# Kernel tuning notes

Measured on AMD Instinct MI355X. Metric: run time of the kernel, lower is better.

The kernel has to match this reference:

```python
import jax, jax.numpy as jnp
import numpy as np

N_NODES = 100000
K = 10
ALPHA = 0.1


def _gcn_norm(ei, n):
    # add self loops (PyG APPNP default: add_self_loops=True, gcn_norm)
    loops = jnp.arange(n, dtype=ei.dtype)
    src = jnp.concatenate([ei[0], loops])
    dst = jnp.concatenate([ei[1], loops])
    ones = jnp.ones(src.shape[0], dtype=jnp.float32)
    deg = jax.ops.segment_sum(ones, dst, num_segments=n)
    dinv = jnp.where(deg > 0, jax.lax.rsqrt(deg), 0.0)
    norm = dinv[src] * dinv[dst]  # [E+N]
    return src, dst, norm


def reference(x, ei, W1, b1, W2, b2):
    n = x.shape[0]
    # MLP encoder (dropout is identity in eval mode)
    h = jax.nn.relu(x @ W1 + b1)
    h = h @ W2 + b2  # [N, out_c]
    src, dst, norm = _gcn_norm(ei, n)
    h0 = h
    for _ in range(K):
        msg = norm[:, None] * h[src]                      # gather [E+N, out_c]
        agg = jax.ops.segment_sum(msg, dst, num_segments=n)  # scatter-add
        h = (1.0 - ALPHA) * agg + ALPHA * h0
    return h


def setup_inputs() -> dict:
    key = jax.random.key(0)
    k1, k2, k3, k4 = jax.random.split(key, 4)
    in_c, hidden, out_c = 512, 256, 64
    E = 3200000
    x = jax.random.normal(k1, (N_NODES, in_c), dtype=jnp.float32)
    ei = jax.random.randint(k2, (2, E), 0, N_NODES, dtype=jnp.int64)
    s1 = 1.0 / np.sqrt(in_c)
    s2 = 1.0 / np.sqrt(hidden)
    W1 = jax.random.uniform(k3, (in_c, hidden), jnp.float32, -s1, s1)
    b1 = jnp.zeros((hidden,), jnp.float32)
    W2 = jax.random.uniform(k4, (hidden, out_c), jnp.float32, -s2, s2)
    b2 = jnp.zeros((out_c,), jnp.float32)
    return {"x": x, "ei": ei, "W1": W1, "b1": b1, "W2": W2, "b2": b2}
```

## Files before the change

### kernel.cpp

```cpp
#include <hip/hip_runtime.h>


typedef unsigned short u16;
typedef unsigned int   u32;
typedef __bf16    bfx8  __attribute__((ext_vector_type(8)));
typedef _Float16  h16x8 __attribute__((ext_vector_type(8)));
typedef float     f32x4 __attribute__((ext_vector_type(4)));

#define CAP 4096
#define EPB 16384
#define NBMAX 1792

__device__ __forceinline__ u16 f2bf(float f) {
    u32 u = __float_as_uint(f);
    u += 0x7fffu + ((u >> 16) & 1u);
    return (u16)(u >> 16);
}


__global__ __launch_bounds__(256) void binscat_kernel(
        const int* __restrict__ src, const int* __restrict__ dst,
        int* __restrict__ gcur, u32* __restrict__ binned, int E, int NB) {
    __shared__ int cnt[NBMAX];
    int tid = threadIdx.x;
#pragma unroll
    for (int j = 0; j < NBMAX / 256; ++j) cnt[tid + j * 256] = 0;
    __syncthreads();
    int e0 = blockIdx.x * EPB;
    for (int r = 0; r < EPB / 256; ++r) {
        int i = e0 + r * 256 + tid;
        if (i < E) atomicAdd(&cnt[dst[i] >> 6], 1);
    }
    __syncthreads();
    for (int j = 0; j < NBMAX / 256; ++j) {
        int b = tid + j * 256;
        if (b < NB) {
            int c = cnt[b];
            cnt[b] = (c > 0) ? atomicAdd(&gcur[b], c) : 0;
        }
    }
    __syncthreads();
    for (int r = 0; r < EPB / 256; ++r) {
        int i = e0 + r * 256 + tid;
        if (i < E) {
            int d = dst[i];
            int s = src[i];
            int bb = d >> 6;
            int p = atomicAdd(&cnt[bb], 1);
            if (p < CAP) binned[(size_t)bb * CAP + p] = ((u32)(d & 63) << 17) | (u32)s;
        }
    }
}


__global__ __launch_bounds__(256) void bucket_scan_kernel(
        const int* __restrict__ gcur, int* __restrict__ bbase,
        int* __restrict__ rp, int N, int NB) {
    __shared__ int tsum[256];
    int tid = threadIdx.x;
    int loc[7];
    int run = 0;
#pragma unroll
    for (int j = 0; j < 7; ++j) {
        int b = tid * 7 + j;
        int v = 0;
        if (b < NB) { v = gcur[b]; if (v > CAP) v = CAP; }
        loc[j] = run;
        run += v;
    }
    tsum[tid] = run;
    __syncthreads();
    for (int off = 1; off < 256; off <<= 1) {
        int t = (tid >= off) ? tsum[tid - off] : 0;
        __syncthreads();
        tsum[tid] += t;
        __syncthreads();
    }
    int texcl = tsum[tid] - run;
#pragma unroll
    for (int j = 0; j < 7; ++j) {
        int b = tid * 7 + j;
        if (b < NB) bbase[b] = texcl + loc[j];
    }
    if (tid == 255) rp[N] = tsum[255];
}


__global__ __launch_bounds__(256) void buildcsr_kernel(
        const u32* __restrict__ binned, const int* __restrict__ gcur,
        const int* __restrict__ bbase, int* __restrict__ rp,
        float* __restrict__ dinv, int* __restrict__ csr, int N) {
    __shared__ u32 eb[CAP];
    __shared__ int lcsr[CAP];
    __shared__ int ncnt[64];
    __shared__ int lcur[64];
    int b = blockIdx.x;
    int tid = threadIdx.x;
    int cnt = gcur[b]; if (cnt > CAP) cnt = CAP;
    int base = bbase[b];
    if (tid < 64) ncnt[tid] = 0;
    __syncthreads();
    for (int idx = tid; idx < cnt; idx += 256) {
        u32 v = binned[(size_t)b * CAP + idx];
        eb[idx] = v;
        atomicAdd(&ncnt[v >> 17], 1);
    }
    __syncthreads();
    if (tid < 64) {
        int c = ncnt[tid];
        int s = c;
#pragma unroll
        for (int off = 1; off < 64; off <<= 1) {
            int t = __shfl_up(s, off);
            if (tid >= off) s += t;
        }
        int excl = s - c;
        lcur[tid] = excl;
        int node = b * 64 + tid;
        if (node < N) {
            rp[node] = base + excl;
            dinv[node] = rsqrtf(1.0f + (float)c);
        }
    }
    __syncthreads();
    for (int idx = tid; idx < cnt; idx += 256) {
        u32 v = eb[idx];
        int p = atomicAdd(&lcur[v >> 17], 1);
        lcsr[p] = (int)(v & 0x1FFFFu);
    }
    __syncthreads();
    for (int idx = tid; idx < cnt; idx += 256)
        csr[base + idx] = lcsr[idx];
}


__global__ void prepw1_kernel(const float* __restrict__ W1, u16* __restrict__ W1t) {
    int id = blockIdx.x * 256 + threadIdx.x;
    int k = id >> 8, n = id & 255;
    W1t[n * 512 + k] = f2bf(W1[id]);
}

__global__ void prepw2_kernel(const float* __restrict__ W2, u16* __restrict__ W2t) {
    int id = blockIdx.x * 256 + threadIdx.x;
    int k = id >> 6, n = id & 63;
    W2t[n * 256 + k] = f2bf(W2[id]);
}


__global__ __launch_bounds__(256) void mlp_kernel(
        const float* __restrict__ x, const u16* __restrict__ W1t,
        const float* __restrict__ b1, const u16* __restrict__ W2t,
        const float* __restrict__ b2, const float* __restrict__ dinv,
        float* __restrict__ h0, _Float16* __restrict__ hA, int N) {
    __shared__ char lds[65536];
    u16* xs  = (u16*)lds;
    u16* w1s = (u16*)(lds + 5120);
    u16* h1s = (u16*)lds;
    u16* w2s = (u16*)(lds + 32768);

    const int tid  = threadIdx.x;
    const int wave = tid >> 6;
    const int lane = tid & 63;
    const int lq   = lane >> 4;
    const int lr   = lane & 15;
    const int blockRow = blockIdx.x * 64;

    f32x4 acc[4][4];
#pragma unroll
    for (int a = 0; a < 4; ++a)
#pragma unroll
        for (int b = 0; b < 4; ++b) acc[a][b] = (f32x4){0.f, 0.f, 0.f, 0.f};

    for (int kk = 0; kk < 512; kk += 32) {
        __syncthreads();
        {
            int r = tid >> 2, c = (tid & 3) << 3;
            int gr = blockRow + r;
            float v[8];
            if (gr < N) {
                const float* p = x + (size_t)gr * 512 + kk + c;
                float4 u0 = *(const float4*)p;
                float4 u1 = *(const float4*)(p + 4);
                v[0]=u0.x; v[1]=u0.y; v[2]=u0.z; v[3]=u0.w;
                v[4]=u1.x; v[5]=u1.y; v[6]=u1.z; v[7]=u1.w;
            } else {
#pragma unroll
                for (int j = 0; j < 8; ++j) v[j] = 0.f;
            }
            u32 pk[4];
#pragma unroll
            for (int j = 0; j < 4; ++j)
                pk[j] = (u32)f2bf(v[2*j]) | ((u32)f2bf(v[2*j+1]) << 16);
            uint4 st = make_uint4(pk[0], pk[1], pk[2], pk[3]);
            *(uint4*)&xs[r * 40 + c] = st;
        }
        {
            const uint4* p = (const uint4*)(W1t + (size_t)tid * 512 + kk);
            uint4* q = (uint4*)&w1s[tid * 40];
            q[0] = p[0]; q[1] = p[1]; q[2] = p[2]; q[3] = p[3];
        }
        __syncthreads();
        bfx8 fa[4], fb[4];
#pragma unroll
        for (int mt = 0; mt < 4; ++mt)
            fa[mt] = *(bfx8*)&xs[(mt * 16 + lr) * 40 + lq * 8];
#pragma unroll
        for (int nt = 0; nt < 4; ++nt)
            fb[nt] = *(bfx8*)&w1s[(wave * 64 + nt * 16 + lr) * 40 + lq * 8];
#pragma unroll
        for (int mt = 0; mt < 4; ++mt)
#pragma unroll
            for (int nt = 0; nt < 4; ++nt)
                acc[mt][nt] = __builtin_amdgcn_mfma_f32_16x16x32_bf16(
                    fa[mt], fb[nt], acc[mt][nt], 0, 0, 0);
    }
    __syncthreads();

#pragma unroll
    for (int nt = 0; nt < 4; ++nt) {
        int col = wave * 64 + nt * 16 + lr;
        float bb = b1[col];
#pragma unroll
        for (int mt = 0; mt < 4; ++mt)
#pragma unroll
            for (int r = 0; r < 4; ++r) {
                int row = mt * 16 + lq * 4 + r;
                float v = acc[mt][nt][r] + bb;
                v = v > 0.f ? v : 0.f;
                h1s[row * 256 + col] = f2bf(v);
            }
    }
    {
        int nn = tid >> 2, seg = (tid & 3) * 64;
        const uint4* p = (const uint4*)(W2t + nn * 256 + seg);
        uint4* q = (uint4*)&w2s[nn * 256 + seg];
#pragma unroll
        for (int j = 0; j < 8; ++j) q[j] = p[j];
    }
    __syncthreads();

    f32x4 acc2[4];
#pragma unroll
    for (int a = 0; a < 4; ++a) acc2[a] = (f32x4){0.f, 0.f, 0.f, 0.f};
    for (int kk = 0; kk < 256; kk += 32) {
        bfx8 a = *(bfx8*)&h1s[(wave * 16 + lr) * 256 + kk + lq * 8];
#pragma unroll
        for (int nt = 0; nt < 4; ++nt) {
            bfx8 b = *(bfx8*)&w2s[(nt * 16 + lr) * 256 + kk + lq * 8];
            acc2[nt] = __builtin_amdgcn_mfma_f32_16x16x32_bf16(a, b, acc2[nt], 0, 0, 0);
        }
    }
#pragma unroll
    for (int nt = 0; nt < 4; ++nt) {
        int col = nt * 16 + lr;
        float bb = b2[col];
#pragma unroll
        for (int r = 0; r < 4; ++r) {
            int row = wave * 16 + lq * 4 + r;
            int gr = blockRow + row;
            if (gr < N) {
                float v = acc2[nt][r] + bb;
                size_t idx = (size_t)gr * 64 + col;
                h0[idx] = v;
                hA[idx] = (_Float16)(v * dinv[gr]);
            }
        }
    }
}


template <typename OUTT>
__global__ __launch_bounds__(256) void prop_kernel(
        const _Float16* __restrict__ hs, const float* __restrict__ h0,
        const float* __restrict__ dinv, const int* __restrict__ rp,
        const int* __restrict__ csr, OUTT* __restrict__ hout, int N) {
    int t = blockIdx.x * 256 + threadIdx.x;
    int i = t >> 3;
    int l = t & 7;
    if (i >= N) return;
    int beg = rp[i], end = rp[i + 1];
    const _Float16* hb = hs + l * 8;
    h16x8 self = *(const h16x8*)(hb + (size_t)i * 64);
    float a[8];
#pragma unroll
    for (int j = 0; j < 8; ++j) a[j] = (float)self[j];
    int e = beg;
    for (; e + 1 < end; e += 2) {
        int s0 = csr[e], s1 = csr[e + 1];
        h16x8 g0 = *(const h16x8*)(hb + (size_t)s0 * 64);
        h16x8 g1 = *(const h16x8*)(hb + (size_t)s1 * 64);
#pragma unroll
        for (int j = 0; j < 8; ++j) a[j] += (float)g0[j];
#pragma unroll
        for (int j = 0; j < 8; ++j) a[j] += (float)g1[j];
    }
    if (e < end) {
        int s0 = csr[e];
        h16x8 g0 = *(const h16x8*)(hb + (size_t)s0 * 64);
#pragma unroll
        for (int j = 0; j < 8; ++j) a[j] += (float)g0[j];
    }
    float dv = dinv[i];
    float c1 = 0.9f * dv;
    const float* h0p = h0 + (size_t)i * 64 + l * 8;
    float o[8];
#pragma unroll
    for (int j = 0; j < 8; ++j) o[j] = fmaf(c1, a[j], 0.1f * h0p[j]);
    if constexpr (sizeof(OUTT) == 2) {
        h16x8 ov;
#pragma unroll
        for (int j = 0; j < 8; ++j) ov[j] = (_Float16)(dv * o[j]);
        *(h16x8*)(hout + (size_t)i * 64 + l * 8) = ov;
    } else {
        float4* q = (float4*)(hout + (size_t)i * 64 + l * 8);
        q[0] = make_float4(o[0], o[1], o[2], o[3]);
        q[1] = make_float4(o[4], o[5], o[6], o[7]);
    }
}


extern "C" void kernel_launch(void* const* d_in, const int* in_sizes, int n_in,
                              void* d_out, int out_size, void* d_ws, size_t ws_size,
                              hipStream_t stream) {
    const float* x  = (const float*)d_in[0];
    const int*   ei = (const int*)d_in[1];
    const float* W1 = (const float*)d_in[2];
    const float* b1 = (const float*)d_in[3];
    const float* W2 = (const float*)d_in[4];
    const float* b2 = (const float*)d_in[5];
    const int N = in_sizes[0] / 512;
    const int E = in_sizes[1] / 2;
    const int NB = (N + 63) / 64;
    const int* src = ei;
    const int* dst = ei + E;

    char* w = (char*)d_ws;
    size_t off = 0;
    auto alloc = [&](size_t bytes) -> char* {
        char* p = w + off;
        off = (off + bytes + 1023) & ~(size_t)1023;
        return p;
    };
    int*      gcur  = (int*)alloc((size_t)NB * 4);
    int*      bbase = (int*)alloc((size_t)NB * 4);
    int*      rp    = (int*)alloc(((size_t)N + 1) * 4);
    float*    dinv  = (float*)alloc((size_t)N * 4);
    int*      csr   = (int*)alloc((size_t)E * 4);
    u32*      binned= (u32*)alloc((size_t)NB * CAP * 4);
    u16*      W1t   = (u16*)alloc(512 * 256 * 2);
    u16*      W2t   = (u16*)alloc(256 * 64 * 2);
    float*    h0    = (float*)alloc((size_t)N * 64 * 4);
    _Float16* hA    = (_Float16*)alloc((size_t)N * 64 * 2);
    _Float16* hB    = (_Float16*)alloc((size_t)N * 64 * 2);

    hipMemsetAsync(gcur, 0, (size_t)NB * 4, stream);
    binscat_kernel<<<(E + EPB - 1) / EPB, 256, 0, stream>>>(src, dst, gcur, binned, E, NB);
    bucket_scan_kernel<<<1, 256, 0, stream>>>(gcur, bbase, rp, N, NB);
    buildcsr_kernel<<<NB, 256, 0, stream>>>(binned, gcur, bbase, rp, dinv, csr, N);
    prepw1_kernel<<<512, 256, 0, stream>>>(W1, W1t);
    prepw2_kernel<<<64, 256, 0, stream>>>(W2, W2t);
    mlp_kernel<<<(N + 63) / 64, 256, 0, stream>>>(x, W1t, b1, W2t, b2, dinv, h0, hA, N);

    const _Float16* pin = hA;
    int grid = (N * 8 + 255) / 256;
    for (int it = 0; it < 9; ++it) {
        _Float16* pout = (it & 1) ? hA : hB;
        prop_kernel<_Float16><<<grid, 256, 0, stream>>>(pin, h0, dinv, rp, csr, pout, N);
        pin = pout;
    }
    prop_kernel<float><<<grid, 256, 0, stream>>>(pin, h0, dinv, rp, csr, (float*)d_out, N);
}
```

Measured before the change: 1.089 ms.

## Sort nodes by degree, double-buffer MLP tiles, store h0 in fp16, unroll gathers

Adds a degree histogram and counting-sort permutation so propagation threads that share a wavefront handle nodes of similar degree, which reduces divergence from uneven neighbour loops. The MLP first-layer loop is double-buffered so global loads for the next K-tile overlap the MFMA work on the current one. W2 is now read directly from global memory instead of being staged in LDS, and the h1 row stride is padded. h0 is stored in fp16, halving its traffic in every propagation pass at some cost in precision. The gather loop is unrolled by four to keep more loads in flight. The permuted node order may hurt locality of the output writes.

```diff
diff --git a/kernel.cpp b/kernel.cpp
--- a/kernel.cpp
+++ b/kernel.cpp
@@ -89,7 +89,8 @@
 __global__ __launch_bounds__(256) void buildcsr_kernel(
         const u32* __restrict__ binned, const int* __restrict__ gcur,
         const int* __restrict__ bbase, int* __restrict__ rp,
-        float* __restrict__ dinv, int* __restrict__ csr, int N) {
+        float* __restrict__ dinv, int* __restrict__ csr,
+        int* __restrict__ dhist, int N) {
     __shared__ u32 eb[CAP];
     __shared__ int lcsr[CAP];
     __shared__ int ncnt[64];
@@ -120,6 +121,8 @@
         if (node < N) {
             rp[node] = base + excl;
             dinv[node] = rsqrtf(1.0f + (float)c);
+            int dg = c > 127 ? 127 : c;
+            atomicAdd(&dhist[dg], 1);
         }
     }
     __syncthreads();
@@ -134,6 +137,44 @@
 }
 
 
+__global__ void dscan_kernel(const int* __restrict__ dhist, int* __restrict__ dcur) {
+    __shared__ int s[128];
+    int tid = threadIdx.x;
+    int v = dhist[tid];
+    s[tid] = v;
+    __syncthreads();
+    for (int off = 1; off < 128; off <<= 1) {
+        int t = (tid >= off) ? s[tid - off] : 0;
+        __syncthreads();
+        s[tid] += t;
+        __syncthreads();
+    }
+    dcur[tid] = s[tid] - v;
+}
+
+__global__ __launch_bounds__(256) void dplace_kernel(
+        const int* __restrict__ rp, int* __restrict__ dcur,
+        int* __restrict__ perm, int N) {
+    __shared__ int cnt[128];
+    __shared__ int base[128];
+    int tid = threadIdx.x;
+    if (tid < 128) cnt[tid] = 0;
+    __syncthreads();
+    int i = blockIdx.x * 256 + tid;
+    int deg = 0, lpos = 0;
+    bool valid = i < N;
+    if (valid) {
+        deg = rp[i + 1] - rp[i];
+        if (deg > 127) deg = 127;
+        lpos = atomicAdd(&cnt[deg], 1);
+    }
+    __syncthreads();
+    if (tid < 128) base[tid] = cnt[tid] ? atomicAdd(&dcur[tid], cnt[tid]) : 0;
+    __syncthreads();
+    if (valid) perm[base[deg] + lpos] = i;
+}
+
+
 __global__ void prepw1_kernel(const float* __restrict__ W1, u16* __restrict__ W1t) {
     int id = blockIdx.x * 256 + threadIdx.x;
     int k = id >> 8, n = id & 255;
@@ -151,12 +192,8 @@
         const float* __restrict__ x, const u16* __restrict__ W1t,
         const float* __restrict__ b1, const u16* __restrict__ W2t,
         const float* __restrict__ b2, const float* __restrict__ dinv,
-        float* __restrict__ h0, _Float16* __restrict__ hA, int N) {
-    __shared__ char lds[65536];
-    u16* xs  = (u16*)lds;
-    u16* w1s = (u16*)(lds + 5120);
-    u16* h1s = (u16*)lds;
-    u16* w2s = (u16*)(lds + 32768);
+        _Float16* __restrict__ h0h, _Float16* __restrict__ hA, int N) {
+    __shared__ __align__(16) char lds[51200];
 
     const int tid  = threadIdx.x;
     const int wave = tid >> 6;
@@ -165,57 +202,72 @@
     const int lr   = lane & 15;
     const int blockRow = blockIdx.x * 64;
 
+    const int sr = tid >> 2;
+    const int sc = (tid & 3) << 3;
+
+    float xv[8];
+    uint4 wv[4];
+    auto load_tile = [&](int ks) {
+        int kk = ks * 32;
+        int gr = blockRow + sr;
+        if (gr < N) {
+            const float* p = x + (size_t)gr * 512 + kk + sc;
+            float4 a0 = *(const float4*)p;
+            float4 a1 = *(const float4*)(p + 4);
+            xv[0]=a0.x; xv[1]=a0.y; xv[2]=a0.z; xv[3]=a0.w;
+            xv[4]=a1.x; xv[5]=a1.y; xv[6]=a1.z; xv[7]=a1.w;
+        } else {
+#pragma unroll
+            for (int j = 0; j < 8; ++j) xv[j] = 0.f;
+        }
+        const uint4* q = (const uint4*)(W1t + (size_t)tid * 512 + kk);
+        wv[0]=q[0]; wv[1]=q[1]; wv[2]=q[2]; wv[3]=q[3];
+    };
+    auto store_tile = [&](int buf) {
+        u16* xsb = (u16*)(lds + buf * 5120);
+        u32 pk[4];
+#pragma unroll
+        for (int j = 0; j < 4; ++j)
+            pk[j] = (u32)f2bf(xv[2*j]) | ((u32)f2bf(xv[2*j+1]) << 16);
+        *(uint4*)&xsb[sr * 40 + sc] = make_uint4(pk[0], pk[1], pk[2], pk[3]);
+        u16* w1b = (u16*)(lds + 10240 + buf * 20480);
+        uint4* qq = (uint4*)&w1b[tid * 40];
+        qq[0]=wv[0]; qq[1]=wv[1]; qq[2]=wv[2]; qq[3]=wv[3];
+    };
+
     f32x4 acc[4][4];
 #pragma unroll
     for (int a = 0; a < 4; ++a)
 #pragma unroll
         for (int b = 0; b < 4; ++b) acc[a][b] = (f32x4){0.f, 0.f, 0.f, 0.f};
 
-    for (int kk = 0; kk < 512; kk += 32) {
-        __syncthreads();
-        {
-            int r = tid >> 2, c = (tid & 3) << 3;
-            int gr = blockRow + r;
-            float v[8];
-            if (gr < N) {
-                const float* p = x + (size_t)gr * 512 + kk + c;
-                float4 u0 = *(const float4*)p;
-                float4 u1 = *(const float4*)(p + 4);
-                v[0]=u0.x; v[1]=u0.y; v[2]=u0.z; v[3]=u0.w;
-                v[4]=u1.x; v[5]=u1.y; v[6]=u1.z; v[7]=u1.w;
-            } else {
-#pragma unroll
-                for (int j = 0; j < 8; ++j) v[j] = 0.f;
-            }
-            u32 pk[4];
-#pragma unroll
-            for (int j = 0; j < 4; ++j)
-                pk[j] = (u32)f2bf(v[2*j]) | ((u32)f2bf(v[2*j+1]) << 16);
-            uint4 st = make_uint4(pk[0], pk[1], pk[2], pk[3]);
-            *(uint4*)&xs[r * 40 + c] = st;
-        }
-        {
-            const uint4* p = (const uint4*)(W1t + (size_t)tid * 512 + kk);
-            uint4* q = (uint4*)&w1s[tid * 40];
-            q[0] = p[0]; q[1] = p[1]; q[2] = p[2]; q[3] = p[3];
-        }
-        __syncthreads();
+    load_tile(0);
+    store_tile(0);
+    __syncthreads();
+    for (int ks = 0; ks < 16; ++ks) {
+        int buf = ks & 1;
+        if (ks < 15) load_tile(ks + 1);
+        const u16* xsb = (const u16*)(lds + buf * 5120);
+        const u16* w1b = (const u16*)(lds + 10240 + buf * 20480);
         bfx8 fa[4], fb[4];
 #pragma unroll
         for (int mt = 0; mt < 4; ++mt)
-            fa[mt] = *(bfx8*)&xs[(mt * 16 + lr) * 40 + lq * 8];
+            fa[mt] = *(const bfx8*)&xsb[(mt * 16 + lr) * 40 + lq * 8];
 #pragma unroll
         for (int nt = 0; nt < 4; ++nt)
-            fb[nt] = *(bfx8*)&w1s[(wave * 64 + nt * 16 + lr) * 40 + lq * 8];
+            fb[nt] = *(const bfx8*)&w1b[(wave * 64 + nt * 16 + lr) * 40 + lq * 8];
 #pragma unroll
         for (int mt = 0; mt < 4; ++mt)
 #pragma unroll
             for (int nt = 0; nt < 4; ++nt)
                 acc[mt][nt] = __builtin_amdgcn_mfma_f32_16x16x32_bf16(
                     fa[mt], fb[nt], acc[mt][nt], 0, 0, 0);
-    }
-    __syncthreads();
-
+        __syncthreads();
+        if (ks < 15) store_tile(buf ^ 1);
+        __syncthreads();
+    }
+
+    u16* h1s = (u16*)lds;
 #pragma unroll
     for (int nt = 0; nt < 4; ++nt) {
         int col = wave * 64 + nt * 16 + lr;
@@ -227,15 +279,8 @@
                 int row = mt * 16 + lq * 4 + r;
                 float v = acc[mt][nt][r] + bb;
                 v = v > 0.f ? v : 0.f;
-                h1s[row * 256 + col] = f2bf(v);
+                h1s[row * 264 + col] = f2bf(v);
             }
-    }
-    {
-        int nn = tid >> 2, seg = (tid & 3) * 64;
-        const uint4* p = (const uint4*)(W2t + nn * 256 + seg);
-        uint4* q = (uint4*)&w2s[nn * 256 + seg];
-#pragma unroll
-        for (int j = 0; j < 8; ++j) q[j] = p[j];
     }
     __syncthreads();
 
@@ -243,10 +288,10 @@
 #pragma unroll
     for (int a = 0; a < 4; ++a) acc2[a] = (f32x4){0.f, 0.f, 0.f, 0.f};
     for (int kk = 0; kk < 256; kk += 32) {
-        bfx8 a = *(bfx8*)&h1s[(wave * 16 + lr) * 256 + kk + lq * 8];
+        bfx8 a = *(const bfx8*)&h1s[(wave * 16 + lr) * 264 + kk + lq * 8];
 #pragma unroll
         for (int nt = 0; nt < 4; ++nt) {
-            bfx8 b = *(bfx8*)&w2s[(nt * 16 + lr) * 256 + kk + lq * 8];
+            bfx8 b = *(const bfx8*)(W2t + (nt * 16 + lr) * 256 + kk + lq * 8);
             acc2[nt] = __builtin_amdgcn_mfma_f32_16x16x32_bf16(a, b, acc2[nt], 0, 0, 0);
         }
     }
@@ -261,8 +306,8 @@
             if (gr < N) {
                 float v = acc2[nt][r] + bb;
                 size_t idx = (size_t)gr * 64 + col;
-                h0[idx] = v;
-                hA[idx] = (_Float16)(v * dinv[gr]);
+                h0h[idx] = (_Float16)v;
+                hA[idx]  = (_Float16)(v * dinv[gr]);
             }
         }
     }
@@ -271,13 +316,15 @@
 
 template <typename OUTT>
 __global__ __launch_bounds__(256) void prop_kernel(
-        const _Float16* __restrict__ hs, const float* __restrict__ h0,
+        const _Float16* __restrict__ hs, const _Float16* __restrict__ h0h,
         const float* __restrict__ dinv, const int* __restrict__ rp,
-        const int* __restrict__ csr, OUTT* __restrict__ hout, int N) {
+        const int* __restrict__ csr, const int* __restrict__ perm,
+        OUTT* __restrict__ hout, int N) {
     int t = blockIdx.x * 256 + threadIdx.x;
-    int i = t >> 3;
+    int slot = t >> 3;
     int l = t & 7;
-    if (i >= N) return;
+    if (slot >= N) return;
+    int i = perm[slot];
     int beg = rp[i], end = rp[i + 1];
     const _Float16* hb = hs + l * 8;
     h16x8 self = *(const h16x8*)(hb + (size_t)i * 64);
@@ -285,16 +332,22 @@
 #pragma unroll
     for (int j = 0; j < 8; ++j) a[j] = (float)self[j];
     int e = beg;
-    for (; e + 1 < end; e += 2) {
-        int s0 = csr[e], s1 = csr[e + 1];
+    for (; e + 3 < end; e += 4) {
+        int s0 = csr[e], s1 = csr[e + 1], s2 = csr[e + 2], s3 = csr[e + 3];
         h16x8 g0 = *(const h16x8*)(hb + (size_t)s0 * 64);
         h16x8 g1 = *(const h16x8*)(hb + (size_t)s1 * 64);
+        h16x8 g2 = *(const h16x8*)(hb + (size_t)s2 * 64);
+        h16x8 g3 = *(const h16x8*)(hb + (size_t)s3 * 64);
 #pragma unroll
         for (int j = 0; j < 8; ++j) a[j] += (float)g0[j];
 #pragma unroll
         for (int j = 0; j < 8; ++j) a[j] += (float)g1[j];
-    }
-    if (e < end) {
+#pragma unroll
+        for (int j = 0; j < 8; ++j) a[j] += (float)g2[j];
+#pragma unroll
+        for (int j = 0; j < 8; ++j) a[j] += (float)g3[j];
+    }
+    for (; e < end; ++e) {
         int s0 = csr[e];
         h16x8 g0 = *(const h16x8*)(hb + (size_t)s0 * 64);
 #pragma unroll
@@ -302,10 +355,11 @@
     }
     float dv = dinv[i];
     float c1 = 0.9f * dv;
-    const float* h0p = h0 + (size_t)i * 64 + l * 8;
+    const _Float16* h0p = h0h + (size_t)i * 64 + l * 8;
+    h16x8 h0v = *(const h16x8*)h0p;
     float o[8];
 #pragma unroll
-    for (int j = 0; j < 8; ++j) o[j] = fmaf(c1, a[j], 0.1f * h0p[j]);
+    for (int j = 0; j < 8; ++j) o[j] = fmaf(c1, a[j], 0.1f * (float)h0v[j]);
     if constexpr (sizeof(OUTT) == 2) {
         h16x8 ov;
 #pragma unroll
@@ -349,24 +403,30 @@
     u32*      binned= (u32*)alloc((size_t)NB * CAP * 4);
     u16*      W1t   = (u16*)alloc(512 * 256 * 2);
     u16*      W2t   = (u16*)alloc(256 * 64 * 2);
-    float*    h0    = (float*)alloc((size_t)N * 64 * 4);
+    _Float16* h0h   = (_Float16*)alloc((size_t)N * 64 * 2);
     _Float16* hA    = (_Float16*)alloc((size_t)N * 64 * 2);
     _Float16* hB    = (_Float16*)alloc((size_t)N * 64 * 2);
+    int*      perm  = (int*)alloc((size_t)N * 4);
+    int*      dhist = (int*)alloc(128 * 4);
+    int*      dcur  = (int*)alloc(128 * 4);
 
     hipMemsetAsync(gcur, 0, (size_t)NB * 4, stream);
+    hipMemsetAsync(dhist, 0, 128 * 4, stream);
     binscat_kernel<<<(E + EPB - 1) / EPB, 256, 0, stream>>>(src, dst, gcur, binned, E, NB);
     bucket_scan_kernel<<<1, 256, 0, stream>>>(gcur, bbase, rp, N, NB);
-    buildcsr_kernel<<<NB, 256, 0, stream>>>(binned, gcur, bbase, rp, dinv, csr, N);
+    buildcsr_kernel<<<NB, 256, 0, stream>>>(binned, gcur, bbase, rp, dinv, csr, dhist, N);
+    dscan_kernel<<<1, 128, 0, stream>>>(dhist, dcur);
+    dplace_kernel<<<(N + 255) / 256, 256, 0, stream>>>(rp, dcur, perm, N);
     prepw1_kernel<<<512, 256, 0, stream>>>(W1, W1t);
     prepw2_kernel<<<64, 256, 0, stream>>>(W2, W2t);
-    mlp_kernel<<<(N + 63) / 64, 256, 0, stream>>>(x, W1t, b1, W2t, b2, dinv, h0, hA, N);
+    mlp_kernel<<<(N + 63) / 64, 256, 0, stream>>>(x, W1t, b1, W2t, b2, dinv, h0h, hA, N);
 
     const _Float16* pin = hA;
     int grid = (N * 8 + 255) / 256;
     for (int it = 0; it < 9; ++it) {
         _Float16* pout = (it & 1) ? hA : hB;
-        prop_kernel<_Float16><<<grid, 256, 0, stream>>>(pin, h0, dinv, rp, csr, pout, N);
+        prop_kernel<_Float16><<<grid, 256, 0, stream>>>(pin, h0h, dinv, rp, csr, perm, pout, N);
         pin = pout;
     }
-    prop_kernel<float><<<grid, 256, 0, stream>>>(pin, h0, dinv, rp, csr, (float*)d_out, N);
-}
+    prop_kernel<float><<<grid, 256, 0, stream>>>(pin, h0h, dinv, rp, csr, perm, (float*)d_out, N);
+}
```

After: 1.363 ms. +25.2%, slower.
